# Performance work log

Measured on AMD Instinct MI355X. Metric: run time of the kernel, lower is better.

The kernel has to match this reference:

```python
import jax, jax.numpy as jnp
import numpy as np

TOKENS = 512
IN_F = 8192
OUT_F = 8192
RANK = 64
NNZ = 8192
QMAX = 127.0  # int8 symmetric


def setup_inputs() -> dict:
    key = jax.random.key(0)
    ks = jax.random.split(key, 12)
    x = jax.random.normal(ks[0], (TOKENS, IN_F), dtype=jnp.float32)
    quantized_weight = jax.random.randint(ks[1], (OUT_F, IN_F), -128, 128, dtype=jnp.int32)
    weight_scale = jax.random.uniform(ks[2], (OUT_F,), minval=0.005, maxval=0.02, dtype=jnp.float32)
    smooth_scales = jax.random.uniform(ks[3], (IN_F,), minval=0.5, maxval=2.0, dtype=jnp.float32)
    act_scale = jnp.array([0.05], dtype=jnp.float32)
    outlier_rows = jax.random.randint(ks[4], (NNZ,), 0, OUT_F, dtype=jnp.int32)
    outlier_cols = jax.random.randint(ks[5], (NNZ,), 0, IN_F, dtype=jnp.int32)
    outlier_vals = jax.random.normal(ks[6], (NNZ,), dtype=jnp.float32) * 0.1
    svd_U = jax.random.normal(ks[7], (OUT_F, RANK), dtype=jnp.float32) * 0.02
    svd_S = jax.random.uniform(ks[8], (RANK,), minval=0.1, maxval=1.0, dtype=jnp.float32)
    svd_V = jax.random.normal(ks[9], (IN_F, RANK), dtype=jnp.float32) * 0.02
    bias = jax.random.normal(ks[10], (OUT_F,), dtype=jnp.float32) * 0.01
    return {"x": x, "quantized_weight": quantized_weight, "weight_scale": weight_scale,
            "smooth_scales": smooth_scales, "act_scale": act_scale,
            "outlier_rows": outlier_rows, "outlier_cols": outlier_cols,
            "outlier_vals": outlier_vals, "svd_U": svd_U, "svd_S": svd_S,
            "svd_V": svd_V, "bias": bias}


def reference(x, quantized_weight, weight_scale, smooth_scales, act_scale,
              outlier_rows, outlier_cols, outlier_vals, svd_U, svd_S, svd_V, bias):
    # SmoothQuant: migrate activation outliers into the weight scales
    x_s = x / smooth_scales  # [T, in]
    # per-tensor symmetric int8 activation fake-quant
    a = act_scale[0]
    x_q = jnp.clip(jnp.round(x_s / a), -QMAX - 1.0, QMAX)
    x_dq = x_q * a  # [T, in]
    # dequantize weight: per-output-channel scale, plus sparse outlier correction
    W = quantized_weight.astype(jnp.float32) * weight_scale[:, None]  # [out, in]
    W = W.at[outlier_rows, outlier_cols].add(outlier_vals)
    # dense quantized matmul
    y = x_dq @ W.T  # [T, out]
    # low-rank SVD residual: x @ (U S V^T)^T = ((x @ V) * S) @ U^T
    y = y + ((x_dq @ svd_V) * svd_S) @ svd_U.T
    return y + bias
```

## Files before the change

kernel.cpp:

```cpp
#include <hip/hip_runtime.h>
#include <hip/hip_bf16.h>

#define TOKENS 512
#define IN_F 8192
#define OUT_F 8192
#define RANK 64
#define NNZ 8192

#define KSPLIT 4
#define KRANGE (IN_F / KSPLIT)
#define BM 512
#define BN 128
#define BK 64
#define NT (KRANGE / BK)

typedef __attribute__((ext_vector_type(8))) short short8;
typedef __attribute__((ext_vector_type(4))) float f32x4;
typedef __attribute__((ext_vector_type(4))) int int4v;

__device__ __forceinline__ unsigned short f2bf(float f) {
  unsigned int u = __builtin_bit_cast(unsigned int, f);
  u += 0x7FFFu + ((u >> 16) & 1u);
  return (unsigned short)(u >> 16);
}
__device__ __forceinline__ float bf2f(unsigned short b) {
  unsigned int u = ((unsigned int)b) << 16;
  return __builtin_bit_cast(float, u);
}

__device__ __forceinline__ void gload_lds16(const void* g, void* l) {
  __builtin_amdgcn_global_load_lds(
      (const __attribute__((address_space(1))) unsigned int*)(g),
      (__attribute__((address_space(3))) unsigned int*)(l), 16, 0, 0);
}

#define WAIT_VM(n) asm volatile("s_waitcnt vmcnt(" #n ")" ::: "memory")
#define WAIT_LGKM0 asm volatile("s_waitcnt lgkmcnt(0)" ::: "memory")
#define SCHED0 __builtin_amdgcn_sched_barrier(0)

__global__ __launch_bounds__(256) void k_quant(const float* __restrict__ x,
                                               const float* __restrict__ smooth,
                                               const float* __restrict__ act,
                                               unsigned short* __restrict__ Abf,
                                               unsigned char* __restrict__ Aq) {
  int idx = blockIdx.x * 256 + threadIdx.x;
  int base = idx * 4;
  int col = base & (IN_F - 1);
  float a = act[0];
  float4 xx = *(const float4*)(x + base);
  float4 ss = *(const float4*)(smooth + col);
  float q0 = fminf(fmaxf(rintf((xx.x / ss.x) / a), -128.f), 127.f);
  float q1 = fminf(fmaxf(rintf((xx.y / ss.y) / a), -128.f), 127.f);
  float q2 = fminf(fmaxf(rintf((xx.z / ss.z) / a), -128.f), 127.f);
  float q3 = fminf(fmaxf(rintf((xx.w / ss.w) / a), -128.f), 127.f);
  ushort4 o;
  o.x = f2bf(q0); o.y = f2bf(q1); o.z = f2bf(q2); o.w = f2bf(q3);
  *(ushort4*)(Abf + base) = o;
  int i0 = (int)q0, i1 = (int)q1, i2 = (int)q2, i3 = (int)q3;
  unsigned int p = (i0 & 0xFF) | ((i1 & 0xFF) << 8) | ((i2 & 0xFF) << 16) |
                   ((unsigned)(i3 & 0xFF) << 24);
  *(unsigned int*)(Aq + base) = p;
}

__global__ __launch_bounds__(256) void k_lr1(const unsigned short* __restrict__ Abf,
                                             const float* __restrict__ V,
                                             const float* __restrict__ S,
                                             const float* __restrict__ act,
                                             float* __restrict__ t) {
  int bid = blockIdx.x;
  int mb = (bid & 3) * 128;
  int kb0 = (bid >> 2) * 512;
  int tid = threadIdx.x, w = tid >> 6, l = tid & 63;
  int lr = l & 15, lg = l >> 4;
  f32x4 acc[2][4] = {};
  for (int ks = 0; ks < 16; ++ks) {
    int kb = kb0 + ks * 32;
    short8 af[2];
#pragma unroll
    for (int fi = 0; fi < 2; ++fi) {
      int row = mb + w * 32 + fi * 16 + lr;
      af[fi] = *(const short8*)(Abf + (size_t)row * IN_F + kb + lg * 8);
    }
    short8 bfr[4];
#pragma unroll
    for (int fj = 0; fj < 4; ++fj) {
      int rk = fj * 16 + lr;
      short8 bv;
#pragma unroll
      for (int j = 0; j < 8; ++j)
        bv[j] = (short)f2bf(V[(size_t)(kb + lg * 8 + j) * RANK + rk]);
      bfr[fj] = bv;
    }
#pragma unroll
    for (int fi = 0; fi < 2; ++fi)
#pragma unroll
      for (int fj = 0; fj < 4; ++fj)
        acc[fi][fj] = __builtin_amdgcn_mfma_f32_16x16x32_bf16(af[fi], bfr[fj], acc[fi][fj], 0, 0, 0);
  }
  float a = act[0];
#pragma unroll
  for (int fi = 0; fi < 2; ++fi)
#pragma unroll
    for (int fj = 0; fj < 4; ++fj) {
      int rk = fj * 16 + lr;
      float sc = a * S[rk];
#pragma unroll
      for (int r = 0; r < 4; ++r) {
        int tok = mb + w * 32 + fi * 16 + lg * 4 + r;
        atomicAdd(t + tok * RANK + rk, acc[fi][fj][r] * sc);
      }
    }
}

__global__ __launch_bounds__(256) void k_lr2(const float* __restrict__ t,
                                             const float* __restrict__ U,
                                             const float* __restrict__ bias,
                                             float* __restrict__ out) {
  int bid = blockIdx.x;
  int mb = (bid & 3) * 128;
  int nb = (bid >> 2) * 128;
  int tid = threadIdx.x, w = tid >> 6, l = tid & 63;
  int lr = l & 15, lg = l >> 4;
  int wm = w >> 1, wn = w & 1;
  f32x4 acc[4][4] = {};
#pragma unroll
  for (int kk = 0; kk < 2; ++kk) {
    short8 af[4], bfr[4];
#pragma unroll
    for (int fi = 0; fi < 4; ++fi) {
      int row = mb + wm * 64 + fi * 16 + lr;
      const float4* tp = (const float4*)(t + (size_t)row * RANK + kk * 32 + lg * 8);
      float4 t0 = tp[0], t1 = tp[1];
      af[fi][0] = f2bf(t0.x); af[fi][1] = f2bf(t0.y);
      af[fi][2] = f2bf(t0.z); af[fi][3] = f2bf(t0.w);
      af[fi][4] = f2bf(t1.x); af[fi][5] = f2bf(t1.y);
      af[fi][6] = f2bf(t1.z); af[fi][7] = f2bf(t1.w);
    }
#pragma unroll
    for (int fj = 0; fj < 4; ++fj) {
      int row = nb + wn * 64 + fj * 16 + lr;
      const float4* up = (const float4*)(U + (size_t)row * RANK + kk * 32 + lg * 8);
      float4 u0 = up[0], u1 = up[1];
      bfr[fj][0] = f2bf(u0.x); bfr[fj][1] = f2bf(u0.y);
      bfr[fj][2] = f2bf(u0.z); bfr[fj][3] = f2bf(u0.w);
      bfr[fj][4] = f2bf(u1.x); bfr[fj][5] = f2bf(u1.y);
      bfr[fj][6] = f2bf(u1.z); bfr[fj][7] = f2bf(u1.w);
    }
#pragma unroll
    for (int fi = 0; fi < 4; ++fi)
#pragma unroll
      for (int fj = 0; fj < 4; ++fj)
        acc[fi][fj] = __builtin_amdgcn_mfma_f32_16x16x32_bf16(af[fi], bfr[fj], acc[fi][fj], 0, 0, 0);
  }
#pragma unroll
  for (int fj = 0; fj < 4; ++fj) {
    int o = nb + wn * 64 + fj * 16 + lr;
    float b = bias[o];
#pragma unroll
    for (int fi = 0; fi < 4; ++fi)
#pragma unroll
      for (int r = 0; r < 4; ++r) {
        int tok = mb + wm * 64 + fi * 16 + lg * 4 + r;
        out[(size_t)tok * OUT_F + o] = b + acc[fi][fj][r];
      }
  }
}

__global__ __launch_bounds__(256) void k_outlier_merge(
    const unsigned short* __restrict__ Abf, const int* __restrict__ rows,
    const int* __restrict__ cols, const float* __restrict__ vals,
    const float* __restrict__ act, const float* __restrict__ wscale,
    const int* __restrict__ part, float* __restrict__ out) {
  __shared__ float accr[OUT_F];
  int tk = blockIdx.x;
  for (int i = threadIdx.x; i < OUT_F; i += 256) accr[i] = 0.f;
  __syncthreads();
  float a = act[0];
  for (int i = threadIdx.x; i < NNZ; i += 256) {
    int r = rows[i], c = cols[i];
    float v = vals[i];
    float xq = bf2f(Abf[(size_t)tk * IN_F + c]);
    atomicAdd(accr + r, a * xq * v);
  }
  __syncthreads();
  float* orow = out + (size_t)tk * OUT_F;
  const int* p0 = part + (size_t)tk * OUT_F;
  const int* p1 = p0 + (size_t)TOKENS * OUT_F;
  const int* p2 = p1 + (size_t)TOKENS * OUT_F;
  const int* p3 = p2 + (size_t)TOKENS * OUT_F;
  for (int i = threadIdx.x * 4; i < OUT_F; i += 1024) {
    int4v s0 = *(const int4v*)(p0 + i);
    int4v s1 = *(const int4v*)(p1 + i);
    int4v s2 = *(const int4v*)(p2 + i);
    int4v s3 = *(const int4v*)(p3 + i);
    float4 ws = *(const float4*)(wscale + i);
    float4 ov = *(const float4*)(orow + i);
    ov.x += accr[i + 0] + (float)(s0[0] + s1[0] + s2[0] + s3[0]) * a * ws.x;
    ov.y += accr[i + 1] + (float)(s0[1] + s1[1] + s2[1] + s3[1]) * a * ws.y;
    ov.z += accr[i + 2] + (float)(s0[2] + s1[2] + s2[2] + s3[2]) * a * ws.z;
    ov.w += accr[i + 3] + (float)(s0[3] + s1[3] + s2[3] + s3[3]) * a * ws.w;
    *(float4*)(orow + i) = ov;
  }
}

__global__ __launch_bounds__(1024, 4) void k_gemm(const unsigned char* __restrict__ Aq,
                                                  const int* __restrict__ W,
                                                  int* __restrict__ part) {
  __shared__ __align__(16) unsigned char As[3][BM * BK];
  __shared__ __align__(16) unsigned char Bs[3][BN * BK];

  int d = blockIdx.x;
  int wg = (d & 7) * 32 + (d >> 3);
  int ks = wg >> 6;
  int nb = wg & 63;
  int kb0 = ks * KRANGE;

  int tid = threadIdx.x, w = tid >> 6, l = tid & 63;
  int lr = l & 15, lg = l >> 4;
  int wm = w >> 1, wn = w & 1;

  int4v acc[4][4] = {};
  int4v wa[2], wb[2];

  const int rW = tid >> 3;
  const int kcW = (tid & 7) * 8;
  const int uW = (kcW >> 4) ^ ((rW >> 1) & 3);
  const int offW = kcW & 15;

  auto LOAD_W = [&](int4v (&wr)[2], int kt) {
    const int* wp = W + (size_t)(nb * BN + rW) * IN_F + kb0 +
                    (kt & (NT - 1)) * BK + kcW;
    wr[0] = *(const int4v*)wp;
    wr[1] = *(const int4v*)(wp + 4);
  };
  auto STAGE_A = [&](int buf, int kt) {
    int kb = kb0 + (kt & (NT - 1)) * BK;
#pragma unroll
    for (int i = 0; i < 2; ++i) {
      int lidx = i * 1024 + w * 64;
      int U = lidx + l;
      int r = U >> 2, up = U & 3;
      int u = up ^ ((r >> 1) & 3);
      gload_lds16(Aq + (size_t)r * IN_F + kb + u * 16, &As[buf][(size_t)lidx * 16]);
    }
  };
  auto DSWRITE_B = [&](int buf, const int4v (&wr)[2]) {
    unsigned int w0 = 0, w1 = 0;
#pragma unroll
    for (int j = 0; j < 4; ++j) w0 |= ((unsigned)(wr[0][j] & 0xFF)) << (8 * j);
#pragma unroll
    for (int j = 0; j < 4; ++j) w1 |= ((unsigned)(wr[1][j] & 0xFF)) << (8 * j);
    uint2 val; val.x = w0; val.y = w1;
    *(uint2*)(&Bs[buf][(size_t)rW * BK + uW * 16 + offW]) = val;
  };
  auto LDFA = [&](int buf, int row) -> int4v {
    int u = lg ^ ((row >> 1) & 3);
    return *(const int4v*)(&As[buf][(size_t)row * BK + u * 16]);
  };
  auto LDFB = [&](int buf, int row) -> int4v {
    int u = lg ^ ((row >> 1) & 3);
    return *(const int4v*)(&Bs[buf][(size_t)row * BK + u * 16]);
  };
  auto COMPUTE = [&](int buf) {
    int4v b0 = LDFB(buf, wn * 64 + 0 * 16 + lr);
    int4v b1 = LDFB(buf, wn * 64 + 1 * 16 + lr);
    int4v b2 = LDFB(buf, wn * 64 + 2 * 16 + lr);
    int4v b3 = LDFB(buf, wn * 64 + 3 * 16 + lr);
    __builtin_amdgcn_s_setprio(1);
#pragma unroll
    for (int fi = 0; fi < 4; ++fi) {
      int4v af = LDFA(buf, wm * 64 + fi * 16 + lr);
      acc[fi][0] = __builtin_amdgcn_mfma_i32_16x16x64_i8(af, b0, acc[fi][0], 0, 0, 0);
      acc[fi][1] = __builtin_amdgcn_mfma_i32_16x16x64_i8(af, b1, acc[fi][1], 0, 0, 0);
      acc[fi][2] = __builtin_amdgcn_mfma_i32_16x16x64_i8(af, b2, acc[fi][2], 0, 0, 0);
      acc[fi][3] = __builtin_amdgcn_mfma_i32_16x16x64_i8(af, b3, acc[fi][3], 0, 0, 0);
    }
    __builtin_amdgcn_s_setprio(0);
  };

  STAGE_A(0, 0);
  LOAD_W(wa, 0);
  STAGE_A(1, 1);
  LOAD_W(wb, 1);
  WAIT_VM(4);
  DSWRITE_B(0, wa);
  WAIT_LGKM0;
  SCHED0;
  __builtin_amdgcn_s_barrier();
  SCHED0;

  int c = 0;
  for (int kt = 0; kt < NT; kt += 2) {
    int c1 = c + 1 == 3 ? 0 : c + 1;
    int c2 = c1 + 1 == 3 ? 0 : c1 + 1;
    STAGE_A(c2, kt + 2);
    LOAD_W(wa, kt + 2);
    COMPUTE(c);
    WAIT_VM(4);
    DSWRITE_B(c1, wb);
    WAIT_LGKM0;
    SCHED0;
    __builtin_amdgcn_s_barrier();
    SCHED0;
    STAGE_A(c, kt + 3);
    LOAD_W(wb, kt + 3);
    COMPUTE(c1);
    WAIT_VM(4);
    DSWRITE_B(c2, wa);
    WAIT_LGKM0;
    SCHED0;
    __builtin_amdgcn_s_barrier();
    SCHED0;
    c = c2;
  }

  int* pp = part + (size_t)ks * TOKENS * OUT_F;
#pragma unroll
  for (int fj = 0; fj < 4; ++fj) {
    int o = nb * BN + wn * 64 + fj * 16 + lr;
#pragma unroll
    for (int fi = 0; fi < 4; ++fi)
#pragma unroll
      for (int rr = 0; rr < 4; ++rr) {
        int tok = wm * 64 + fi * 16 + lg * 4 + rr;
        pp[(size_t)tok * OUT_F + o] = acc[fi][fj][rr];
      }
  }
}

extern "C" void kernel_launch(void* const* d_in, const int* in_sizes, int n_in,
                              void* d_out, int out_size, void* d_ws, size_t ws_size,
                              hipStream_t stream) {
  const float* x = (const float*)d_in[0];
  const int* W = (const int*)d_in[1];
  const float* wscale = (const float*)d_in[2];
  const float* smooth = (const float*)d_in[3];
  const float* act = (const float*)d_in[4];
  const int* orow = (const int*)d_in[5];
  const int* ocol = (const int*)d_in[6];
  const float* oval = (const float*)d_in[7];
  const float* U = (const float*)d_in[8];
  const float* S = (const float*)d_in[9];
  const float* V = (const float*)d_in[10];
  const float* bias = (const float*)d_in[11];
  float* out = (float*)d_out;

  unsigned short* Abf = (unsigned short*)d_ws;
  unsigned char* Aq = (unsigned char*)d_ws + (size_t)TOKENS * IN_F * 2;
  float* t = (float*)((char*)d_ws + (size_t)TOKENS * IN_F * 3);
  int* part = (int*)((char*)d_ws + (size_t)TOKENS * IN_F * 3 +
                     (size_t)TOKENS * RANK * 4);

  hipMemsetAsync(t, 0, TOKENS * RANK * sizeof(float), stream);
  k_quant<<<(TOKENS * IN_F / 4) / 256, 256, 0, stream>>>(x, smooth, act, Abf, Aq);
  k_gemm<<<256, 1024, 0, stream>>>(Aq, W, part);
  k_lr1<<<64, 256, 0, stream>>>(Abf, V, S, act, t);
  k_lr2<<<256, 256, 0, stream>>>(t, U, bias, out);
  k_outlier_merge<<<TOKENS, 256, 0, stream>>>(Abf, orow, ocol, oval, act,
                                              wscale, part, out);
}
```

Measured before the change: 185.6 us.

## Remap GEMM warps to 32x128 tiles and replace low-rank atomics with split partials

The int8 GEMM now gives each of the 16 warps a 32-token by 128-output tile. Each warp stages its own A rows into a private LDS slice and reuses two A fragments across eight B fragments, instead of the earlier 64x64 warp tile. Separately, k_lr1 writes per-K-split partial sums to 16 buffers, and k_lr2 reduces them. This removes the atomics and the memset. The warp remap raises B LDS reads per warp, and the split adds workspace and extra reads in k_lr2.

After: 203.1 us. 1.09x slower.

```diff
diff --git a/kernel.cpp b/kernel.cpp
--- a/kernel.cpp
+++ b/kernel.cpp
@@ -13,6 +13,7 @@
 #define BN 128
 #define BK 64
 #define NT (KRANGE / BK)
+#define LRSPLIT 16
 
 typedef __attribute__((ext_vector_type(8))) short short8;
 typedef __attribute__((ext_vector_type(4))) float f32x4;
@@ -69,7 +70,8 @@
                                              float* __restrict__ t) {
   int bid = blockIdx.x;
   int mb = (bid & 3) * 128;
-  int kb0 = (bid >> 2) * 512;
+  int ksp = bid >> 2;
+  int kb0 = ksp * 512;
   int tid = threadIdx.x, w = tid >> 6, l = tid & 63;
   int lr = l & 15, lg = l >> 4;
   f32x4 acc[2][4] = {};
@@ -98,6 +100,7 @@
         acc[fi][fj] = __builtin_amdgcn_mfma_f32_16x16x32_bf16(af[fi], bfr[fj], acc[fi][fj], 0, 0, 0);
   }
   float a = act[0];
+  float* tk = t + (size_t)ksp * TOKENS * RANK;
 #pragma unroll
   for (int fi = 0; fi < 2; ++fi)
 #pragma unroll
@@ -107,7 +110,7 @@
 #pragma unroll
       for (int r = 0; r < 4; ++r) {
         int tok = mb + w * 32 + fi * 16 + lg * 4 + r;
-        atomicAdd(t + tok * RANK + rk, acc[fi][fj][r] * sc);
+        tk[(size_t)tok * RANK + rk] = acc[fi][fj][r] * sc;
       }
     }
 }
@@ -129,8 +132,14 @@
 #pragma unroll
     for (int fi = 0; fi < 4; ++fi) {
       int row = mb + wm * 64 + fi * 16 + lr;
-      const float4* tp = (const float4*)(t + (size_t)row * RANK + kk * 32 + lg * 8);
-      float4 t0 = tp[0], t1 = tp[1];
+      size_t off = (size_t)row * RANK + kk * 32 + lg * 8;
+      float4 t0 = {0, 0, 0, 0}, t1 = {0, 0, 0, 0};
+      for (int s = 0; s < LRSPLIT; ++s) {
+        const float4* tp = (const float4*)(t + (size_t)s * TOKENS * RANK + off);
+        float4 u0 = tp[0], u1 = tp[1];
+        t0.x += u0.x; t0.y += u0.y; t0.z += u0.z; t0.w += u0.w;
+        t1.x += u1.x; t1.y += u1.y; t1.z += u1.z; t1.w += u1.w;
+      }
       af[fi][0] = f2bf(t0.x); af[fi][1] = f2bf(t0.y);
       af[fi][2] = f2bf(t0.z); af[fi][3] = f2bf(t0.w);
       af[fi][4] = f2bf(t1.x); af[fi][5] = f2bf(t1.y);
@@ -206,7 +215,7 @@
 __global__ __launch_bounds__(1024, 4) void k_gemm(const unsigned char* __restrict__ Aq,
                                                   const int* __restrict__ W,
                                                   int* __restrict__ part) {
-  __shared__ __align__(16) unsigned char As[3][BM * BK];
+  __shared__ __align__(16) unsigned char As[3][16][32 * BK];
   __shared__ __align__(16) unsigned char Bs[3][BN * BK];
 
   int d = blockIdx.x;
@@ -217,9 +226,8 @@
 
   int tid = threadIdx.x, w = tid >> 6, l = tid & 63;
   int lr = l & 15, lg = l >> 4;
-  int wm = w >> 1, wn = w & 1;
-
-  int4v acc[4][4] = {};
+
+  int4v acc[2][8] = {};
   int4v wa[2], wb[2];
 
   const int rW = tid >> 3;
@@ -237,11 +245,11 @@
     int kb = kb0 + (kt & (NT - 1)) * BK;
 #pragma unroll
     for (int i = 0; i < 2; ++i) {
-      int lidx = i * 1024 + w * 64;
-      int U = lidx + l;
-      int r = U >> 2, up = U & 3;
-      int u = up ^ ((r >> 1) & 3);
-      gload_lds16(Aq + (size_t)r * IN_F + kb + u * 16, &As[buf][(size_t)lidx * 16]);
+      int u = i * 64 + l;
+      int r = u >> 2, up = u & 3;
+      int us = up ^ ((r >> 1) & 3);
+      gload_lds16(Aq + (size_t)(w * 32 + r) * IN_F + kb + us * 16,
+                  &As[buf][w][(size_t)(i * 64) * 16]);
     }
   };
   auto DSWRITE_B = [&](int buf, const int4v (&wr)[2]) {
@@ -255,25 +263,21 @@
   };
   auto LDFA = [&](int buf, int row) -> int4v {
     int u = lg ^ ((row >> 1) & 3);
-    return *(const int4v*)(&As[buf][(size_t)row * BK + u * 16]);
+    return *(const int4v*)(&As[buf][w][(size_t)row * BK + u * 16]);
   };
   auto LDFB = [&](int buf, int row) -> int4v {
     int u = lg ^ ((row >> 1) & 3);
     return *(const int4v*)(&Bs[buf][(size_t)row * BK + u * 16]);
   };
   auto COMPUTE = [&](int buf) {
-    int4v b0 = LDFB(buf, wn * 64 + 0 * 16 + lr);
-    int4v b1 = LDFB(buf, wn * 64 + 1 * 16 + lr);
-    int4v b2 = LDFB(buf, wn * 64 + 2 * 16 + lr);
-    int4v b3 = LDFB(buf, wn * 64 + 3 * 16 + lr);
+    int4v af0 = LDFA(buf, lr);
+    int4v af1 = LDFA(buf, 16 + lr);
     __builtin_amdgcn_s_setprio(1);
 #pragma unroll
-    for (int fi = 0; fi < 4; ++fi) {
-      int4v af = LDFA(buf, wm * 64 + fi * 16 + lr);
-      acc[fi][0] = __builtin_amdgcn_mfma_i32_16x16x64_i8(af, b0, acc[fi][0], 0, 0, 0);
-      acc[fi][1] = __builtin_amdgcn_mfma_i32_16x16x64_i8(af, b1, acc[fi][1], 0, 0, 0);
-      acc[fi][2] = __builtin_amdgcn_mfma_i32_16x16x64_i8(af, b2, acc[fi][2], 0, 0, 0);
-      acc[fi][3] = __builtin_amdgcn_mfma_i32_16x16x64_i8(af, b3, acc[fi][3], 0, 0, 0);
+    for (int fj = 0; fj < 8; ++fj) {
+      int4v b = LDFB(buf, fj * 16 + lr);
+      acc[0][fj] = __builtin_amdgcn_mfma_i32_16x16x64_i8(af0, b, acc[0][fj], 0, 0, 0);
+      acc[1][fj] = __builtin_amdgcn_mfma_i32_16x16x64_i8(af1, b, acc[1][fj], 0, 0, 0);
     }
     __builtin_amdgcn_s_setprio(0);
   };
@@ -316,13 +320,13 @@
 
   int* pp = part + (size_t)ks * TOKENS * OUT_F;
 #pragma unroll
-  for (int fj = 0; fj < 4; ++fj) {
-    int o = nb * BN + wn * 64 + fj * 16 + lr;
-#pragma unroll
-    for (int fi = 0; fi < 4; ++fi)
+  for (int fj = 0; fj < 8; ++fj) {
+    int o = nb * BN + fj * 16 + lr;
+#pragma unroll
+    for (int fi = 0; fi < 2; ++fi)
 #pragma unroll
       for (int rr = 0; rr < 4; ++rr) {
-        int tok = wm * 64 + fi * 16 + lg * 4 + rr;
+        int tok = w * 32 + fi * 16 + lg * 4 + rr;
         pp[(size_t)tok * OUT_F + o] = acc[fi][fj][rr];
       }
   }
@@ -349,9 +353,8 @@
   unsigned char* Aq = (unsigned char*)d_ws + (size_t)TOKENS * IN_F * 2;
   float* t = (float*)((char*)d_ws + (size_t)TOKENS * IN_F * 3);
   int* part = (int*)((char*)d_ws + (size_t)TOKENS * IN_F * 3 +
-                     (size_t)TOKENS * RANK * 4);
-
-  hipMemsetAsync(t, 0, TOKENS * RANK * sizeof(float), stream);
+                     (size_t)LRSPLIT * TOKENS * RANK * 4);
+
   k_quant<<<(TOKENS * IN_F / 4) / 256, 256, 0, stream>>>(x, smooth, act, Abf, Aq);
   k_gemm<<<256, 1024, 0, stream>>>(Aq, W, part);
   k_lr1<<<64, 256, 0, stream>>>(Abf, V, S, act, t);
```
